# Kernel tuning notes

Measured on AMD Instinct MI355X. Metric: run time of the kernel, lower is better.

Reference implementation:

```python
import jax, jax.numpy as jnp
import numpy as np


def _h(s):
    # Step function: 0 where s > 0, else 1 (zero gradient everywhere).
    return jnp.where(s > 0, 0.0, 1.0).astype(s.dtype)


def setup_inputs() -> dict:
    key = jax.random.key(0)
    k1, k2, k3 = jax.random.split(key, 3)
    B, T = 4096, 2048
    x = jax.random.normal(k1, (B, T, 1), dtype=jnp.float32)
    out_prev = jax.random.normal(k2, (B, 1, 1), dtype=jnp.float32)
    lstm_outs = jax.random.normal(k3, (B, T, 4), dtype=jnp.float32)
    return {"x": x, "out_prev": out_prev, "lstm_outs": lstm_outs}


def reference(x, out_prev, lstm_outs):
    # x: [B, T, 1], out_prev: [B, 1, 1] (only first step used), lstm_outs: [B, T, 4]
    xT = jnp.swapaxes(x, 0, 1)          # [T, B, 1]
    wT = jnp.swapaxes(lstm_outs, 0, 1)  # [T, B, 4]

    def step(prev, inputs):
        # prev: [B, 1]
        xt, wt = inputs                  # [B, 1], [B, 4]
        m_lo = wt[:, 0:1]
        m_up = wt[:, 1:2]
        c_lo = wt[:, 2:3]
        c_up = wt[:, 3:4]
        # h() arguments use detached weights in the original (grad is zero through
        # the step function anyway); stop_gradient kept for faithfulness.
        m_lo_d = jax.lax.stop_gradient(m_lo)
        m_up_d = jax.lax.stop_gradient(m_up)
        c_lo_d = jax.lax.stop_gradient(c_lo)
        c_up_d = jax.lax.stop_gradient(c_up)
        f1 = _h((m_lo_d * xt + m_lo_d * c_lo_d - prev) / m_lo_d)
        f2 = _h((prev - m_up_d * xt - m_up_d * c_up_d) / m_up_d)
        out = (m_lo * xt * f1 + m_lo * c_lo * f1
               + m_up * xt * f2 + m_up * c_up * f2
               + prev * (1.0 - f1) * (1.0 - f2))
        return out, out

    init = out_prev[:, 0, :]             # [B, 1]
    _, outs = jax.lax.scan(step, init, (xT, wT))  # outs: [T, B, 1]
    custom_output = jnp.swapaxes(outs, 0, 1)      # [B, T, 1]
    # Original also returns (lstm_outs, 0, 0, 0) passthrough; main output is below.
    return custom_output
```

## Files before the change

### kernel.cpp

```cpp
#include <hip/hip_runtime.h>


#define C 64
#define NCH 32
#define NTB 4
#define RS 129
#define SLOT (16 * RS)

#define CFENCE() asm volatile("" ::: "memory")

__global__ __launch_bounds__(192) void pc_scan(
    const float* __restrict__ x, const float* __restrict__ p0,
    const float4* __restrict__ lstm4, float* __restrict__ out,
    int B, int T) {
#pragma clang fp contract(off)
  __shared__ float4 tile[NTB][SLOT];
  __shared__ int stg[NCH][2];
  __shared__ int scanned;

  const int tid = threadIdx.x;
  const int b0 = blockIdx.x * 16;
  float4* out4 = reinterpret_cast<float4*>(out);
  (void)B;

  for (int i = tid; i < 2 * NCH; i += 192) ((int*)stg)[i] = 0;
  if (tid == 0) scanned = 0;
  __syncthreads();

  if (tid >= 64) {
    const int q = tid - 64;
    const int pj = q >> 3;
    const int pk = q & 7;
    const int w = q >> 6;
    const bool lead = (q & 63) == 0;

    float4 L00, L01, L02, L03, L04, L05, L06, L07;
    float4 L10, L11, L12, L13, L14, L15, L16, L17;
    float x00, x01, x02, x03, x04, x05, x06, x07;
    float x10, x11, x12, x13, x14, x15, x16, x17;

#define ISSUE(S, CH)                                                    \
  {                                                                     \
    size_t rb = (size_t)(b0 + pj) * T + (size_t)(CH) * C;               \
    const float4* lp = lstm4 + rb + pk;                                 \
    const float* xp = x + rb + pk;                                      \
    L##S##0 = lp[0];  L##S##1 = lp[8];  L##S##2 = lp[16];               \
    L##S##3 = lp[24]; L##S##4 = lp[32]; L##S##5 = lp[40];               \
    L##S##6 = lp[48]; L##S##7 = lp[56];                                 \
    x##S##0 = xp[0];  x##S##1 = xp[8];  x##S##2 = xp[16];               \
    x##S##3 = xp[24]; x##S##4 = xp[32]; x##S##5 = xp[40];               \
    x##S##6 = xp[48]; x##S##7 = xp[56];                                 \
  }

#define STAGE_ELT(LV, XV, TW, OFF)                                      \
  {                                                                     \
    float4 wv = LV;                       \
    float xv = XV;                                                      \
    float a1 = wv.x * xv, a2 = wv.x * wv.z;                             \
    float L1v = a1 + a2;                                                \
    unsigned s1m = __float_as_uint(wv.x) & 0x80000000u;                 \
    float L1f = __uint_as_float(__float_as_uint(L1v) ^ s1m);            \
    float a3 = wv.y * xv, a4 = wv.y * wv.w;                             \
    unsigned f2m = (__float_as_uint(wv.y) & 0x80000000u) ^ 0x80000000u; \
    float a3f = __uint_as_float(__float_as_uint(a3) ^ f2m);             \
    float a4f = __uint_as_float(__float_as_uint(a4) ^ f2m);             \
    float V01 = a3 + a4;                                                \
    float V11 = (L1v + a3) + a4;                                        \
    (TW)[OFF] = make_float4(__uint_as_float(s1m), L1f,                  \
                            __uint_as_float(f2m), a3f);                 \
    (TW)[(OFF) + 1] = make_float4(a4f, V11, V01, L1v);                  \
  }

#define STAGE(S, BUF)                                                   \
  {                                                                     \
    float4* tw = &tile[BUF][pj * RS + 2 * pk];                          \
    STAGE_ELT(L##S##0, x##S##0, tw, 0)                                  \
    STAGE_ELT(L##S##1, x##S##1, tw, 16)                                 \
    STAGE_ELT(L##S##2, x##S##2, tw, 32)                                 \
    STAGE_ELT(L##S##3, x##S##3, tw, 48)                                 \
    STAGE_ELT(L##S##4, x##S##4, tw, 64)                                 \
    STAGE_ELT(L##S##5, x##S##5, tw, 80)                                 \
    STAGE_ELT(L##S##6, x##S##6, tw, 96)                                 \
    STAGE_ELT(L##S##7, x##S##7, tw, 112)                                \
  }

#define PWAIT(TGT)                                                      \
  while (*(volatile int*)&scanned < (TGT)) __builtin_amdgcn_s_sleep(1); \
  CFENCE();

    ISSUE(0, 0)
    ISSUE(1, 1)

    for (int k = 0; k < NCH; k += 2) {
      PWAIT(k - 3)
      STAGE(0, k & 3)
      CFENCE();
      if (lead) *(volatile int*)&stg[k][w] = 1;
      if (k + 2 < NCH) ISSUE(0, k + 2)
      PWAIT(k - 2)
      STAGE(1, (k + 1) & 3)
      CFENCE();
      if (lead) *(volatile int*)&stg[k + 1][w] = 1;
      if (k + 3 < NCH) ISSUE(1, k + 3)
    }
  } else if (tid < 16) {
    const int row = tid;
    float p = p0[b0 + row];
    float4* op = out4 + (((size_t)(b0 + row) * T) >> 2);
    const float4* base0 = &tile[0][row * RS];
    const float4* slotb = base0;
    const float4* gp;

    float4 rA0E, rA1E, rA2E, rA3E, rA4E, rA5E, rA6E, rA7E;
    float4 rB0E, rB1E, rB2E, rB3E, rB4E, rB5E, rB6E, rB7E;
    float4 rA0O, rA1O, rA2O, rA3O, rA4O, rA5O, rA6O, rA7O;
    float4 rB0O, rB1O, rB2O, rB3O, rB4O, rB5O, rB6O, rB7O;

#define CWAIT(CC)                                                       \
  for (;;) {                                                            \
    int fa = *(volatile int*)&stg[CC][0];                               \
    int fb = *(volatile int*)&stg[CC][1];                               \
    if (fa + fb == 2) break;                                            \
  }                                                                     \
  CFENCE();

#define LOADG(S, P)                                                     \
  rA0##S = (P)[0];  rB0##S = (P)[1];  rA1##S = (P)[2];  rB1##S = (P)[3];\
  rA2##S = (P)[4];  rB2##S = (P)[5];  rA3##S = (P)[6];  rB3##S = (P)[7];\
  rA4##S = (P)[8];  rB4##S = (P)[9];  rA5##S = (P)[10]; rB5##S = (P)[11];\
  rA6##S = (P)[12]; rB6##S = (P)[13]; rA7##S = (P)[14]; rB7##S = (P)[15];

#define RSTEP(S, I, OV)                                                 \
  {                                                                     \
    float4 A = rA##I##S;                                                \
    float4 Bv = rB##I##S;                                               \
    unsigned pu = __float_as_uint(p);                                   \
    float pf = __uint_as_float(pu ^ __float_as_uint(A.x));              \
    bool c1 = pf >= A.y;                                                \
    float pp = __uint_as_float(pu ^ __float_as_uint(A.z));              \
    float qv = pp - A.w;                                                \
    bool c2 = qv >= Bv.x;                                               \
    float i1 = c1 ? Bv.y : Bv.z;                                        \
    float i2 = c1 ? Bv.w : p;                                           \
    p = c2 ? i1 : i2;                                                   \
    OV = p;                                                             \
  }

#define BODY(CUR, NXT, CG, LAST)                                        \
  {                                                                     \
    const int cg_ = (CG);                                               \
    if (!(LAST)) {                                                      \
      int ncg = cg_ + 1;                                                \
      const float4* np;                                                 \
      if ((ncg & 7) == 0) {                                             \
        int nc = ncg >> 3;                                              \
        CWAIT(nc)                                                       \
        slotb = ((nc & 3) == 0) ? base0 : (slotb + SLOT);               \
        np = slotb;                                                     \
      } else {                                                          \
        np = gp + 16;                                                   \
      }                                                                 \
      LOADG(NXT, np)                                                    \
      gp = np;                                                          \
    }                                                                   \
    float4 ov0, ov1;                                                    \
    RSTEP(CUR, 0, ov0.x) RSTEP(CUR, 1, ov0.y)                           \
    RSTEP(CUR, 2, ov0.z) RSTEP(CUR, 3, ov0.w)                           \
    RSTEP(CUR, 4, ov1.x) RSTEP(CUR, 5, ov1.y)                           \
    RSTEP(CUR, 6, ov1.z) RSTEP(CUR, 7, ov1.w)                           \
    op[0] = ov0;                                                        \
    op[1] = ov1;                                                        \
    op += 2;                                                            \
    if (((cg_) & 7) == 7 && row == 0)                                   \
      *(volatile int*)&scanned = (cg_ >> 3) + 1;                        \
  }

    CWAIT(0)
    gp = base0;
    LOADG(E, gp)
    for (int it = 0; it < 127; ++it) {
      BODY(E, O, 2 * it, 0)
      BODY(O, E, 2 * it + 1, 0)
    }
    BODY(E, O, 254, 0)
    BODY(O, E, 255, 1)
  }
}

extern "C" void kernel_launch(void* const* d_in, const int* in_sizes, int n_in,
                              void* d_out, int out_size, void* d_ws, size_t ws_size,
                              hipStream_t stream) {
  const float* x = (const float*)d_in[0];
  const float* op = (const float*)d_in[1];
  const float4* lstm = (const float4*)d_in[2];
  int B = in_sizes[1];
  int T = in_sizes[0] / B;
  hipLaunchKernelGGL(pc_scan, dim3(B / 16), dim3(192), 0, stream,
                     x, op, lstm, (float*)d_out, B, T);
}
```

Before: 248.1 us.

## Stage scan outputs in LDS and flush coalesced by producer warps

The scanning threads (one row each) now write outputs into a 4-deep LDS output staging buffer instead of issuing strided global stores. The producer threads then read each finished chunk back and write it to global memory as coalesced float4 stores, gated by the scanned counter. The coefficient tile is split into separate A/B arrays with 3 buffers instead of 4, which fits the new output buffer in shared memory. In exchange, prefetch slack shrinks by one chunk, producer threads take on store work, and the flush depends on correctly ordered LDS handoff.

```diff
diff --git a/kernel.cpp b/kernel.cpp
--- a/kernel.cpp
+++ b/kernel.cpp
@@ -3,9 +3,10 @@
 
 #define C 64
 #define NCH 32
-#define NTB 4
-#define RS 129
-#define SLOT (16 * RS)
+#define NTB 3
+#define NOB 4
+#define TS 65
+#define XS 68
 
 #define CFENCE() asm volatile("" ::: "memory")
 
@@ -14,7 +15,9 @@
     const float4* __restrict__ lstm4, float* __restrict__ out,
     int B, int T) {
 #pragma clang fp contract(off)
-  __shared__ float4 tile[NTB][SLOT];
+  __shared__ float4 tileA[NTB][16 * TS];
+  __shared__ float4 tileB[NTB][16 * TS];
+  __shared__ float ostg[NOB][16 * XS];
   __shared__ int stg[NCH][2];
   __shared__ int scanned;
 
@@ -29,9 +32,9 @@
 
   if (tid >= 64) {
     const int q = tid - 64;
-    const int pj = q >> 3;
+    const int pj = (q >> 3) & 15;
     const int pk = q & 7;
-    const int w = q >> 6;
+    const int w = (tid >> 6) - 1;
     const bool lead = (q & 63) == 0;
 
     float4 L00, L01, L02, L03, L04, L05, L06, L07;
@@ -52,7 +55,7 @@
     x##S##6 = xp[48]; x##S##7 = xp[56];                                 \
   }
 
-#define STAGE_ELT(LV, XV, TW, OFF)                                      \
+#define STAGE_ELT(LV, XV, SS, BUF)                                      \
   {                                                                     \
     float4 wv = LV;                       \
     float xv = XV;                                                      \
@@ -66,22 +69,30 @@
     float a4f = __uint_as_float(__float_as_uint(a4) ^ f2m);             \
     float V01 = a3 + a4;                                                \
     float V11 = (L1v + a3) + a4;                                        \
-    (TW)[OFF] = make_float4(__uint_as_float(s1m), L1f,                  \
-                            __uint_as_float(f2m), a3f);                 \
-    (TW)[(OFF) + 1] = make_float4(a4f, V11, V01, L1v);                  \
+    tileA[BUF][pj * TS + (SS)] =                                        \
+        make_float4(__uint_as_float(s1m), L1f, __uint_as_float(f2m), a3f); \
+    tileB[BUF][pj * TS + (SS)] = make_float4(a4f, V11, V01, L1v);       \
   }
 
 #define STAGE(S, BUF)                                                   \
   {                                                                     \
-    float4* tw = &tile[BUF][pj * RS + 2 * pk];                          \
-    STAGE_ELT(L##S##0, x##S##0, tw, 0)                                  \
-    STAGE_ELT(L##S##1, x##S##1, tw, 16)                                 \
-    STAGE_ELT(L##S##2, x##S##2, tw, 32)                                 \
-    STAGE_ELT(L##S##3, x##S##3, tw, 48)                                 \
-    STAGE_ELT(L##S##4, x##S##4, tw, 64)                                 \
-    STAGE_ELT(L##S##5, x##S##5, tw, 80)                                 \
-    STAGE_ELT(L##S##6, x##S##6, tw, 96)                                 \
-    STAGE_ELT(L##S##7, x##S##7, tw, 112)                                \
+    STAGE_ELT(L##S##0, x##S##0, pk,      BUF)                           \
+    STAGE_ELT(L##S##1, x##S##1, pk + 8,  BUF)                           \
+    STAGE_ELT(L##S##2, x##S##2, pk + 16, BUF)                           \
+    STAGE_ELT(L##S##3, x##S##3, pk + 24, BUF)                           \
+    STAGE_ELT(L##S##4, x##S##4, pk + 32, BUF)                           \
+    STAGE_ELT(L##S##5, x##S##5, pk + 40, BUF)                           \
+    STAGE_ELT(L##S##6, x##S##6, pk + 48, BUF)                           \
+    STAGE_ELT(L##S##7, x##S##7, pk + 56, BUF)                           \
+  }
+
+#define FLUSH(CP, OB)                                                   \
+  {                                                                     \
+    float4 v0 = *(const float4*)&ostg[OB][pj * XS + 8 * pk];            \
+    float4 v1 = *(const float4*)&ostg[OB][pj * XS + 8 * pk + 4];        \
+    size_t ob = ((size_t)(b0 + pj) * T + (size_t)(CP) * C) >> 2;        \
+    out4[ob + 2 * pk] = v0;                                             \
+    out4[ob + 2 * pk + 1] = v1;                                         \
   }
 
 #define PWAIT(TGT)                                                      \
@@ -92,24 +103,29 @@
     ISSUE(1, 1)
 
     for (int k = 0; k < NCH; k += 2) {
-      PWAIT(k - 3)
-      STAGE(0, k & 3)
+      PWAIT(k - 2)
+      STAGE(0, k % NTB)
       CFENCE();
       if (lead) *(volatile int*)&stg[k][w] = 1;
       if (k + 2 < NCH) ISSUE(0, k + 2)
-      PWAIT(k - 2)
-      STAGE(1, (k + 1) & 3)
+      if (k >= 3) FLUSH(k - 3, (k - 3) & 3)
+      PWAIT(k - 1)
+      STAGE(1, (k + 1) % NTB)
       CFENCE();
       if (lead) *(volatile int*)&stg[k + 1][w] = 1;
       if (k + 3 < NCH) ISSUE(1, k + 3)
+      if (k >= 2) FLUSH(k - 2, (k - 2) & 3)
+    }
+    for (int j = NCH - 3; j < NCH; ++j) {
+      PWAIT(j + 1)
+      FLUSH(j, j & 3)
     }
   } else if (tid < 16) {
     const int row = tid;
     float p = p0[b0 + row];
-    float4* op = out4 + (((size_t)(b0 + row) * T) >> 2);
-    const float4* base0 = &tile[0][row * RS];
-    const float4* slotb = base0;
-    const float4* gp;
+    const float4* pA;
+    const float4* pB;
+    float* od;
 
     float4 rA0E, rA1E, rA2E, rA3E, rA4E, rA5E, rA6E, rA7E;
     float4 rB0E, rB1E, rB2E, rB3E, rB4E, rB5E, rB6E, rB7E;
@@ -124,11 +140,11 @@
   }                                                                     \
   CFENCE();
 
-#define LOADG(S, P)                                                     \
-  rA0##S = (P)[0];  rB0##S = (P)[1];  rA1##S = (P)[2];  rB1##S = (P)[3];\
-  rA2##S = (P)[4];  rB2##S = (P)[5];  rA3##S = (P)[6];  rB3##S = (P)[7];\
-  rA4##S = (P)[8];  rB4##S = (P)[9];  rA5##S = (P)[10]; rB5##S = (P)[11];\
-  rA6##S = (P)[12]; rB6##S = (P)[13]; rA7##S = (P)[14]; rB7##S = (P)[15];
+#define LOADG(S, PA, PB)                                                \
+  rA0##S = (PA)[0]; rA1##S = (PA)[1]; rA2##S = (PA)[2]; rA3##S = (PA)[3];\
+  rA4##S = (PA)[4]; rA5##S = (PA)[5]; rA6##S = (PA)[6]; rA7##S = (PA)[7];\
+  rB0##S = (PB)[0]; rB1##S = (PB)[1]; rB2##S = (PB)[2]; rB3##S = (PB)[3];\
+  rB4##S = (PB)[4]; rB5##S = (PB)[5]; rB6##S = (PB)[6]; rB7##S = (PB)[7];
 
 #define RSTEP(S, I, OV)                                                 \
   {                                                                     \
@@ -151,33 +167,39 @@
     const int cg_ = (CG);                                               \
     if (!(LAST)) {                                                      \
       int ncg = cg_ + 1;                                                \
-      const float4* np;                                                 \
       if ((ncg & 7) == 0) {                                             \
         int nc = ncg >> 3;                                              \
         CWAIT(nc)                                                       \
-        slotb = ((nc & 3) == 0) ? base0 : (slotb + SLOT);               \
-        np = slotb;                                                     \
-      } else {                                                          \
-        np = gp + 16;                                                   \
+        pA = &tileA[nc % NTB][row * TS];                                \
+        pB = &tileB[nc % NTB][row * TS];                                \
       }                                                                 \
-      LOADG(NXT, np)                                                    \
-      gp = np;                                                          \
+      LOADG(NXT, pA, pB)                                                \
+      pA += 8;                                                          \
+      pB += 8;                                                          \
     }                                                                   \
     float4 ov0, ov1;                                                    \
     RSTEP(CUR, 0, ov0.x) RSTEP(CUR, 1, ov0.y)                           \
     RSTEP(CUR, 2, ov0.z) RSTEP(CUR, 3, ov0.w)                           \
     RSTEP(CUR, 4, ov1.x) RSTEP(CUR, 5, ov1.y)                           \
     RSTEP(CUR, 6, ov1.z) RSTEP(CUR, 7, ov1.w)                           \
-    op[0] = ov0;                                                        \
-    op[1] = ov1;                                                        \
-    op += 2;                                                            \
-    if (((cg_) & 7) == 7 && row == 0)                                   \
-      *(volatile int*)&scanned = (cg_ >> 3) + 1;                        \
+    *(float4*)&od[0] = ov0;                                             \
+    *(float4*)&od[4] = ov1;                                             \
+    if ((cg_ & 7) == 7) {                                               \
+      CFENCE();                                                         \
+      if (row == 0) *(volatile int*)&scanned = (cg_ >> 3) + 1;          \
+      od = &ostg[((cg_ >> 3) + 1) & 3][row * XS];                       \
+    } else {                                                            \
+      od += 8;                                                          \
+    }                                                                   \
   }
 
     CWAIT(0)
-    gp = base0;
-    LOADG(E, gp)
+    pA = &tileA[0][row * TS];
+    pB = &tileB[0][row * TS];
+    od = &ostg[0][row * XS];
+    LOADG(E, pA, pB)
+    pA += 8;
+    pB += 8;
     for (int it = 0; it < 127; ++it) {
       BODY(E, O, 2 * it, 0)
       BODY(O, E, 2 * it + 1, 0)
```

After: 240.1 us. 3.2% less time.
